# Kernel optimization log

Hardware: AMD Instinct MI355X
Metric: run time of the kernel (lower is better)

Reference implementation:

```python
import jax, jax.numpy as jnp
import numpy as np

N, C, W_DIM, H_DIM = 2, 256, 64, 64
HEADS = 4
DH = C // HEADS  # per-head dim for Q,K,V projections
EPS = 1e-5


def _layernorm(x, w, b):
    mu = jnp.mean(x, axis=-1, keepdims=True)
    var = jnp.var(x, axis=-1, keepdims=True)
    return (x - mu) * jax.lax.rsqrt(var + EPS) * w + b


def setup_inputs() -> dict:
    key = jax.random.key(0)
    ks = jax.random.split(key, 12)
    s = 1.0 / np.sqrt(C)
    return {
        "x": jax.random.normal(ks[0], (N, C, W_DIM, H_DIM), dtype=jnp.float32),
        "ln1_w": jnp.ones((C,), jnp.float32),
        "ln1_b": jnp.zeros((C,), jnp.float32),
        # per-head projection weights, laid out for x @ W: [heads, C, DH]
        "WQ": jax.random.normal(ks[1], (HEADS, C, DH), jnp.float32) * s,
        "WK": jax.random.normal(ks[2], (HEADS, C, DH), jnp.float32) * s,
        "WV": jax.random.normal(ks[3], (HEADS, C, DH), jnp.float32) * s,
        "ln2_w": jnp.ones((C,), jnp.float32),
        "ln2_b": jnp.zeros((C,), jnp.float32),
        "W1": jax.random.normal(ks[4], (C, C), jnp.float32) * s,
        "b1": jnp.zeros((C,), jnp.float32),
        "W2": jax.random.normal(ks[5], (C, C), jnp.float32) * s,
        "b2": jnp.zeros((C,), jnp.float32),
    }


def reference(x, ln1_w, ln1_b, WQ, WK, WV, ln2_w, ln2_b, W1, b1, W2, b2):
    n, c, w, h = x.shape
    s = w * h
    # 'n c w h -> n (w h) c'
    r = x.reshape(n, c, s).transpose(0, 2, 1)          # [n, s, c]
    norm = _layernorm(r, ln1_w, ln1_b)
    # all heads at once (original loops over heads)
    Q = jnp.einsum('nsc,hcd->nhsd', norm, WQ)
    K = jnp.einsum('nsc,hcd->nhsd', norm, WK)
    V = jnp.einsum('nsc,hcd->nhsd', norm, WV)
    # scale is 1/sqrt(seq_len) per original (keys.shape[1])
    y = jnp.einsum('nhqd,nhkd->nhqk', Q, K) / jnp.sqrt(jnp.float32(s))
    # QUIRK: softmax over dim=1 of [n, q, k] => the QUERY axis (axis=2 here)
    z = jax.nn.softmax(y, axis=2)
    attn = jnp.einsum('nhqk,nhkd->nhqd', z, V)         # [n, h, s, dh]
    attn_cat = attn.transpose(0, 2, 1, 3).reshape(n, s, c)
    out = attn_cat + r
    out = _layernorm(out, ln2_w, ln2_b)
    out = jax.nn.gelu(out @ W1 + b1, approximate=False) @ W2 + b2
    out = out + attn_cat
    # 'n (w h) c -> n c w h'
    return out.transpose(0, 2, 1).reshape(n, c, w, h)
```

## Files before the change

### kernel.cpp

```cpp
#include <hip/hip_runtime.h>
#include <math.h>

#define SEQ 4096
#define CH  256
#define NHT 8
#define DHD 64

#define QSCALE 0.0225421092f

using bf16x8 = __attribute__((ext_vector_type(8))) short;
using f32x4  = __attribute__((ext_vector_type(4))) float;
typedef unsigned short u16;
typedef unsigned int   u32;

__device__ __forceinline__ u16 f2bf(float f) {
    u32 u = __float_as_uint(f);
    u = (u + 0x7fffu + ((u >> 16) & 1u)) >> 16;
    return (u16)u;
}
__device__ __forceinline__ float bf2f(u16 h) {
    return __uint_as_float(((u32)h) << 16);
}
__device__ __forceinline__ float fexp2(float x) {
    return __builtin_amdgcn_exp2f(x);
}

__global__ __launch_bounds__(256) void k_prep(const float* __restrict__ x,
                                              const float* __restrict__ ln1w,
                                              const float* __restrict__ ln1b,
                                              const float* __restrict__ WQ,
                                              const float* __restrict__ WK,
                                              const float* __restrict__ WV,
                                              const float* __restrict__ W1,
                                              const float* __restrict__ W2,
                                              u16* __restrict__ norm,
                                              u16* __restrict__ BtQKV,
                                              u16* __restrict__ W1t,
                                              u16* __restrict__ W2t)
{
    __shared__ float tile[32][257];
    __shared__ float mu[32], rs[32];
    int bid = blockIdx.x;
    int t = threadIdx.x;
    if (bid < 1280) {
        int id = bid * 256 + t;
        if (id < 768 * 256) {
            int j = id >> 8, c = id & 255;
            int which = j >> 8, h = (j >> 6) & 3, d = j & 63;
            const float* W = (which == 0) ? WQ : (which == 1) ? WK : WV;
            BtQKV[id] = f2bf(W[(h * 256 + c) * 64 + d]);
        } else if (id < 768 * 256 + 65536) {
            int jj = id - 768 * 256;
            int j = jj >> 8, c = jj & 255;
            W1t[jj] = f2bf(W1[c * 256 + j]);
        } else if (id < 768 * 256 + 2 * 65536) {
            int jj = id - 768 * 256 - 65536;
            int j = jj >> 8, c = jj & 255;
            W2t[jj] = f2bf(W2[c * 256 + j]);
        }
        return;
    }
    int b2i = bid - 1280;
    int n = b2i >> 7, s0 = (b2i & 127) * 32;
    int sl = t & 31, cg = t >> 5;
    for (int cc = 0; cc < 256; cc += 8) {
        int c = cc + cg;
        tile[sl][c] = x[(n * 256 + c) * SEQ + s0 + sl];
    }
    __syncthreads();
    int wv = t >> 6, l = t & 63;
    for (int rr = 0; rr < 8; rr++) {
        int s = wv * 8 + rr;
        float a0 = tile[s][l], a1 = tile[s][l + 64], a2 = tile[s][l + 128], a3 = tile[s][l + 192];
        float sm = a0 + a1 + a2 + a3;
        float sq = a0 * a0 + a1 * a1 + a2 * a2 + a3 * a3;
        for (int off = 32; off; off >>= 1) { sm += __shfl_xor(sm, off); sq += __shfl_xor(sq, off); }
        if (l == 0) {
            float m = sm * (1.f / 256.f);
            mu[s] = m;
            rs[s] = rsqrtf(sq * (1.f / 256.f) - m * m + 1e-5f);
        }
    }
    __syncthreads();
    float ww = ln1w[t], bb = ln1b[t];
    for (int s = 0; s < 32; s++) {
        float v = (tile[s][t] - mu[s]) * rs[s] * ww + bb;
        norm[(n * SEQ + s0 + s) * 256 + t] = f2bf(v);
    }
}

__global__ __launch_bounds__(256) void k_qkv(const u16* __restrict__ norm,
                                             const u16* __restrict__ Bt,
                                             u16* __restrict__ Qo,
                                             u16* __restrict__ Ko,
                                             u16* __restrict__ Vto)
{
    int m0 = blockIdx.x * 64, j0 = blockIdx.y * 128;
    int t = threadIdx.x, w = t >> 6, lane = t & 63, quad = lane >> 4, l16 = lane & 15;
    const u16* Ap = norm + (long)(m0 + w * 16 + l16) * 256;
    const u16* Bp = Bt + (long)j0 * 256;
    f32x4 z = {0.f, 0.f, 0.f, 0.f};
    f32x4 acc[8];
    #pragma unroll
    for (int j = 0; j < 8; j++) acc[j] = z;
    #pragma unroll
    for (int kc = 0; kc < 8; kc++) {
        bf16x8 a = *(const bf16x8*)&Ap[kc * 32 + quad * 8];
        #pragma unroll
        for (int j = 0; j < 8; j++) {
            bf16x8 b = *(const bf16x8*)&Bp[(long)(j * 16 + l16) * 256 + kc * 32 + quad * 8];
            acc[j] = __builtin_amdgcn_mfma_f32_16x16x32_bf16(a, b, acc[j], 0, 0, 0);
        }
    }
    #pragma unroll
    for (int j = 0; j < 8; j++) {
        int col = j0 + j * 16 + l16;
        int which = col >> 8, h = (col >> 6) & 3, d = col & 63;
        int m = m0 + w * 16 + quad * 4;
        int n = m >> 12, s = m & 4095;
        if (which == 2) {
            u16 h0 = f2bf(acc[j][0]), h1 = f2bf(acc[j][1]);
            u16 h2_ = f2bf(acc[j][2]), h3 = f2bf(acc[j][3]);
            uint2 pk;
            pk.x = (u32)h0 | ((u32)h1 << 16);
            pk.y = (u32)h2_ | ((u32)h3 << 16);
            *(uint2*)&Vto[((long)(n * 4 + h) * 64 + d) * SEQ + s] = pk;
        } else {
            u16* dst = (which == 0) ? Qo : Ko;
            float sc = (which == 0) ? QSCALE : 1.0f;
            #pragma unroll
            for (int r = 0; r < 4; r++)
                dst[((n * 4 + h) * SEQ + s + r) * 64 + d] = f2bf(acc[j][r] * sc);
        }
    }
}

__global__ __launch_bounds__(256) void k_pass1(const u16* __restrict__ Q,
                                               const u16* __restrict__ Km,
                                               float* __restrict__ D4)
{
    __shared__ float Dred[128];
    int nh = blockIdx.y, k0 = blockIdx.x * 128, qc = blockIdx.z;
    const u16* Qh = Q + (long)nh * SEQ * 64;
    const u16* Kh = Km + (long)nh * SEQ * 64;
    int t = threadIdx.x, w = t >> 6, lane = t & 63, quad = lane >> 4, l16 = lane & 15;
    bf16x8 Kf[8][2];
    #pragma unroll
    for (int i = 0; i < 8; i++) {
        Kf[i][0] = *(const bf16x8*)&Kh[(k0 + i * 16 + l16) * 64 + quad * 8];
        Kf[i][1] = *(const bf16x8*)&Kh[(k0 + i * 16 + l16) * 64 + 32 + quad * 8];
    }
    if (t < 128) Dred[t] = 0.f;
    f32x4 z = {0.f, 0.f, 0.f, 0.f};
    float Dacc[8][4] = {};
    const int qw0 = qc * 1024 + w * 256;
    bf16x8 b0 = *(const bf16x8*)&Qh[(qw0 + l16) * 64 + quad * 8];
    bf16x8 b1 = *(const bf16x8*)&Qh[(qw0 + l16) * 64 + 32 + quad * 8];
    for (int step = 0; step < 16; step++) {
        int q = qw0 + step * 16;
        bf16x8 n0, n1;
        if (step < 15) {
            n0 = *(const bf16x8*)&Qh[(q + 16 + l16) * 64 + quad * 8];
            n1 = *(const bf16x8*)&Qh[(q + 16 + l16) * 64 + 32 + quad * 8];
        }
        #pragma unroll
        for (int i = 0; i < 8; i++) {
            f32x4 acc = z;
            acc = __builtin_amdgcn_mfma_f32_16x16x32_bf16(Kf[i][0], b0, acc, 0, 0, 0);
            acc = __builtin_amdgcn_mfma_f32_16x16x32_bf16(Kf[i][1], b1, acc, 0, 0, 0);
            #pragma unroll
            for (int r = 0; r < 4; r++) Dacc[i][r] += fexp2(acc[r]);
        }
        b0 = n0; b1 = n1;
    }
    #pragma unroll
    for (int i = 0; i < 8; i++)
        #pragma unroll
        for (int r = 0; r < 4; r++) {
            float v = Dacc[i][r];
            v += __shfl_xor(v, 1); v += __shfl_xor(v, 2);
            v += __shfl_xor(v, 4); v += __shfl_xor(v, 8);
            Dacc[i][r] = v;
        }
    __syncthreads();
    if (l16 == 0) {
        #pragma unroll
        for (int i = 0; i < 8; i++)
            #pragma unroll
            for (int r = 0; r < 4; r++)
                atomicAdd(&Dred[i * 16 + quad * 4 + r], Dacc[i][r]);
    }
    __syncthreads();
    if (t < 128) D4[((long)(qc * NHT + nh)) * SEQ + k0 + t] = Dred[t];
}

__global__ __launch_bounds__(256) void k_pass2(const u16* __restrict__ Q,
                                               const u16* __restrict__ Km,
                                               const u16* __restrict__ Vt,
                                               const float* __restrict__ D4,
                                               float* __restrict__ acat2)
{
    __shared__ __align__(16) unsigned char smem[34816];
    u16 (*lP)[64][36] = (u16(*)[64][36])smem;
    float* Lk = (float*)(smem + 18432);
    float (*SA)[68] = (float(*)[68])smem;
    float (*SB)[68] = (float(*)[68])(smem + 17408);

    int nh = blockIdx.y, q0 = blockIdx.x * 64, kcid = blockIdx.z;
    int n = nh >> 2, h = nh & 3;
    const u16* Qh = Q + (long)nh * SEQ * 64;
    const u16* Kh = Km + (long)nh * SEQ * 64;
    const u16* Vh = Vt + (long)nh * 64 * SEQ;
    int t = threadIdx.x, w = t >> 6, lane = t & 63, quad = lane >> 4, l16 = lane & 15;
    const int kw0 = kcid * 2048 + w * 512;
    const int klw = w * 512;

    {
        const float* Dp = D4 + (long)nh * SEQ + kcid * 2048;
        const long QS = (long)NHT * SEQ;
        #pragma unroll
        for (int off = 0; off < 8; off++) {
            int kl = off * 256 + t;
            float s = Dp[kl] + Dp[QS + kl] + Dp[2 * QS + kl] + Dp[3 * QS + kl];
            Lk[kl] = __log2f(s);
        }
    }
    bf16x8 Qf[4][2];
    #pragma unroll
    for (int jq = 0; jq < 4; jq++)
        #pragma unroll
        for (int ch = 0; ch < 2; ch++)
            Qf[jq][ch] = *(const bf16x8*)&Qh[(q0 + jq * 16 + l16) * 64 + ch * 32 + quad * 8];
    bf16x8 kA[2][2];
    #pragma unroll
    for (int ksub = 0; ksub < 2; ksub++) {
        kA[ksub][0] = *(const bf16x8*)&Kh[(kw0 + ksub * 16 + l16) * 64 + quad * 8];
        kA[ksub][1] = *(const bf16x8*)&Kh[(kw0 + ksub * 16 + l16) * 64 + 32 + quad * 8];
    }
    f32x4 z = {0.f, 0.f, 0.f, 0.f};
    f32x4 accO[4][4];
    #pragma unroll
    for (int jq = 0; jq < 4; jq++)
        #pragma unroll
        for (int jd = 0; jd < 4; jd++) accO[jq][jd] = z;
    __syncthreads();

    uint2 pk[2][4];
    {
        f32x4 Lv[2];
        #pragma unroll
        for (int ksub = 0; ksub < 2; ksub++)
            Lv[ksub] = *(const f32x4*)&Lk[klw + ksub * 16 + quad * 4];
        #pragma unroll
        for (int ksub = 0; ksub < 2; ksub++)
            #pragma unroll
            for (int jq = 0; jq < 4; jq++) {
                f32x4 acc = z;
                acc = __builtin_amdgcn_mfma_f32_16x16x32_bf16(kA[ksub][0], Qf[jq][0], acc, 0, 0, 0);
                acc = __builtin_amdgcn_mfma_f32_16x16x32_bf16(kA[ksub][1], Qf[jq][1], acc, 0, 0, 0);
                u32 e0 = __float_as_uint(fexp2(acc[0] - Lv[ksub][0]));
                u32 e1 = __float_as_uint(fexp2(acc[1] - Lv[ksub][1]));
                u32 e2 = __float_as_uint(fexp2(acc[2] - Lv[ksub][2]));
                u32 e3 = __float_as_uint(fexp2(acc[3] - Lv[ksub][3]));
                pk[ksub][jq].x = __builtin_amdgcn_perm(e1, e0, 0x07060302u);
                pk[ksub][jq].y = __builtin_amdgcn_perm(e3, e2, 0x07060302u);
            }
    }
    #pragma unroll
    for (int ksub = 0; ksub < 2; ksub++) {
        kA[ksub][0] = *(const bf16x8*)&Kh[(kw0 + 32 + ksub * 16 + l16) * 64 + quad * 8];
        kA[ksub][1] = *(const bf16x8*)&Kh[(kw0 + 32 + ksub * 16 + l16) * 64 + 32 + quad * 8];
    }
    bf16x8 vb[4];
    #pragma unroll
    for (int jd = 0; jd < 4; jd++)
        vb[jd] = *(const bf16x8*)&Vh[(jd * 16 + l16) * SEQ + kw0 + quad * 8];

    for (int i = 0; i < 16; i++) {
        int k0 = kw0 + i * 32;
        #pragma unroll
        for (int ksub = 0; ksub < 2; ksub++)
            #pragma unroll
            for (int jq = 0; jq < 4; jq++)
                *(uint2*)&lP[w][jq * 16 + l16][ksub * 16 + quad * 4] = pk[ksub][jq];
        if (i < 15) {
            f32x4 Lv[2];
            #pragma unroll
            for (int ksub = 0; ksub < 2; ksub++)
                Lv[ksub] = *(const f32x4*)&Lk[klw + (i + 1) * 32 + ksub * 16 + quad * 4];
            #pragma unroll
            for (int ksub = 0; ksub < 2; ksub++)
                #pragma unroll
                for (int jq = 0; jq < 4; jq++) {
                    f32x4 acc = z;
                    acc = __builtin_amdgcn_mfma_f32_16x16x32_bf16(kA[ksub][0], Qf[jq][0], acc, 0, 0, 0);
                    acc = __builtin_amdgcn_mfma_f32_16x16x32_bf16(kA[ksub][1], Qf[jq][1], acc, 0, 0, 0);
                    u32 e0 = __float_as_uint(fexp2(acc[0] - Lv[ksub][0]));
                    u32 e1 = __float_as_uint(fexp2(acc[1] - Lv[ksub][1]));
                    u32 e2 = __float_as_uint(fexp2(acc[2] - Lv[ksub][2]));
                    u32 e3 = __float_as_uint(fexp2(acc[3] - Lv[ksub][3]));
                    pk[ksub][jq].x = __builtin_amdgcn_perm(e1, e0, 0x07060302u);
                    pk[ksub][jq].y = __builtin_amdgcn_perm(e3, e2, 0x07060302u);
                }
            if (i < 14) {
                #pragma unroll
                for (int ksub = 0; ksub < 2; ksub++) {
                    kA[ksub][0] = *(const bf16x8*)&Kh[(k0 + 64 + ksub * 16 + l16) * 64 + quad * 8];
                    kA[ksub][1] = *(const bf16x8*)&Kh[(k0 + 64 + ksub * 16 + l16) * 64 + 32 + quad * 8];
                }
            }
        }
        #pragma unroll
        for (int jq = 0; jq < 4; jq++) {
            bf16x8 pa = *(const bf16x8*)&lP[w][jq * 16 + l16][quad * 8];
            #pragma unroll
            for (int jd = 0; jd < 4; jd++)
                accO[jq][jd] = __builtin_amdgcn_mfma_f32_16x16x32_bf16(pa, vb[jd], accO[jq][jd], 0, 0, 0);
        }
        if (i < 15) {
            #pragma unroll
            for (int jd = 0; jd < 4; jd++)
                vb[jd] = *(const bf16x8*)&Vh[(jd * 16 + l16) * SEQ + k0 + 32 + quad * 8];
        }
    }
    __syncthreads();
    if (w >= 2) {
        float (*S)[68] = (w == 2) ? SA : SB;
        #pragma unroll
        for (int jq = 0; jq < 4; jq++)
            #pragma unroll
            for (int jd = 0; jd < 4; jd++)
                #pragma unroll
                for (int r = 0; r < 4; r++)
                    S[jq * 16 + quad * 4 + r][jd * 16 + l16] = accO[jq][jd][r];
    }
    __syncthreads();
    if (w < 2) {
        float (*S)[68] = (w == 0) ? SA : SB;
        #pragma unroll
        for (int jq = 0; jq < 4; jq++)
            #pragma unroll
            for (int jd = 0; jd < 4; jd++)
                #pragma unroll
                for (int r = 0; r < 4; r++) {
                    float v = accO[jq][jd][r] + S[jq * 16 + quad * 4 + r][jd * 16 + l16];
                    S[jq * 16 + quad * 4 + r][jd * 16 + l16] = v;
                }
    }
    __syncthreads();
    float* dst = acat2 + (long)kcid * 8192 * 256;
    #pragma unroll
    for (int p = 0; p < 4; p++) {
        int row = p * 16 + (t >> 4);
        int ch = (t & 15) * 4;
        float4 va = *(float4*)&SA[row][ch];
        float4 vb2 = *(float4*)&SB[row][ch];
        float4 o = make_float4(va.x + vb2.x, va.y + vb2.y, va.z + vb2.z, va.w + vb2.w);
        *(float4*)&dst[((long)n * SEQ + q0 + row) * 256 + h * 64 + ch] = o;
    }
}

__global__ __launch_bounds__(256) void k_tail(const float* __restrict__ x,
                                              const float* __restrict__ acat2,
                                              const float* __restrict__ lnw,
                                              const float* __restrict__ lnb,
                                              const u16* __restrict__ W1t,
                                              const float* __restrict__ b1v,
                                              const u16* __restrict__ W2t,
                                              const float* __restrict__ b2v,
                                              float* __restrict__ out)
{
    __shared__ __align__(16) unsigned char smem[16448];
    float (*tile)[257] = (float(*)[257])smem;
    u16 (*lT)[264] = (u16(*)[264])smem;
    __shared__ float mu[16], rs[16];
    __shared__ __align__(16) u16 lH[16][264];

    const long STRIDE = (long)8192 * 256;
    int m0 = blockIdx.x * 16;
    int n = m0 >> 12, s0 = m0 & 4095;
    int t = threadIdx.x, w = t >> 6, lane = t & 63, quad = lane >> 4, l16 = lane & 15;

    {
        int sl = t & 15, cg = t >> 4;
        for (int cc = 0; cc < 256; cc += 16) {
            int c = cc + cg;
            tile[sl][c] = x[(n * 256 + c) * SEQ + s0 + sl];
        }
    }
    __syncthreads();
    for (int s = 0; s < 16; s++) {
        long idx = (long)(m0 + s) * 256 + t;
        tile[s][t] += acat2[idx] + acat2[idx + STRIDE];
    }
    __syncthreads();
    {
        int l = t & 63;
        for (int rr = 0; rr < 4; rr++) {
            int s = w * 4 + rr;
            float a0 = tile[s][l], a1 = tile[s][l + 64], a2 = tile[s][l + 128], a3 = tile[s][l + 192];
            float sm = a0 + a1 + a2 + a3;
            float sq = a0 * a0 + a1 * a1 + a2 * a2 + a3 * a3;
            for (int off = 32; off; off >>= 1) { sm += __shfl_xor(sm, off); sq += __shfl_xor(sq, off); }
            if (l == 0) {
                float m = sm * (1.f / 256.f);
                mu[s] = m;
                rs[s] = rsqrtf(sq * (1.f / 256.f) - m * m + 1e-5f);
            }
        }
    }
    __syncthreads();
    {
        float ww = lnw[t], bb = lnb[t];
        for (int s = 0; s < 16; s++)
            lH[s][t] = f2bf((tile[s][t] - mu[s]) * rs[s] * ww + bb);
    }
    __syncthreads();

    f32x4 z = {0.f, 0.f, 0.f, 0.f};
    f32x4 acc1[4];
    #pragma unroll
    for (int js = 0; js < 4; js++) acc1[js] = z;
    #pragma unroll
    for (int kc = 0; kc < 8; kc++) {
        bf16x8 b = *(const bf16x8*)&lH[l16][kc * 32 + quad * 8];
        #pragma unroll
        for (int js = 0; js < 4; js++) {
            bf16x8 a = *(const bf16x8*)&W1t[(long)(w * 64 + js * 16 + l16) * 256 + kc * 32 + quad * 8];
            acc1[js] = __builtin_amdgcn_mfma_f32_16x16x32_bf16(a, b, acc1[js], 0, 0, 0);
        }
    }
    #pragma unroll
    for (int js = 0; js < 4; js++) {
        u32 e[4];
        #pragma unroll
        for (int r = 0; r < 4; r++) {
            int j = w * 64 + js * 16 + quad * 4 + r;
            float v = acc1[js][r] + b1v[j];
            float g = 0.5f * v * (1.f + erff(v * 0.70710678118f));
            u32 u = __float_as_uint(g);
            e[r] = u + 0x7fffu + ((u >> 16) & 1u);
        }
        uint2 pk;
        pk.x = __builtin_amdgcn_perm(e[1], e[0], 0x07060302u);
        pk.y = __builtin_amdgcn_perm(e[3], e[2], 0x07060302u);
        *(uint2*)&lT[l16][w * 64 + js * 16 + quad * 4] = pk;
    }
    __syncthreads();
    f32x4 acc2[4];
    #pragma unroll
    for (int cs = 0; cs < 4; cs++) acc2[cs] = z;
    #pragma unroll
    for (int kc = 0; kc < 8; kc++) {
        bf16x8 pa = *(const bf16x8*)&lT[l16][kc * 32 + quad * 8];
        #pragma unroll
        for (int cs = 0; cs < 4; cs++) {
            bf16x8 wb = *(const bf16x8*)&W2t[(long)(w * 64 + cs * 16 + l16) * 256 + kc * 32 + quad * 8];
            acc2[cs] = __builtin_amdgcn_mfma_f32_16x16x32_bf16(pa, wb, acc2[cs], 0, 0, 0);
        }
    }
    #pragma unroll
    for (int cs = 0; cs < 4; cs++) {
        int c = w * 64 + cs * 16 + l16;
        float bj = b2v[c];
        float vv[4];
        #pragma unroll
        for (int r = 0; r < 4; r++) {
            long idx = (long)(m0 + quad * 4 + r) * 256 + c;
            vv[r] = acc2[cs][r] + bj + acat2[idx] + acat2[idx + STRIDE];
        }
        float4 o = make_float4(vv[0], vv[1], vv[2], vv[3]);
        *(float4*)&out[((long)n * 256 + c) * SEQ + s0 + quad * 4] = o;
    }
}

extern "C" void kernel_launch(void* const* d_in, const int* in_sizes, int n_in,
                              void* d_out, int out_size, void* d_ws, size_t ws_size,
                              hipStream_t stream) {
    const float* x    = (const float*)d_in[0];
    const float* ln1w = (const float*)d_in[1];
    const float* ln1b = (const float*)d_in[2];
    const float* WQ   = (const float*)d_in[3];
    const float* WK   = (const float*)d_in[4];
    const float* WV   = (const float*)d_in[5];
    const float* ln2w = (const float*)d_in[6];
    const float* ln2b = (const float*)d_in[7];
    const float* W1   = (const float*)d_in[8];
    const float* b1   = (const float*)d_in[9];
    const float* W2   = (const float*)d_in[10];
    const float* b2   = (const float*)d_in[11];
    float* out = (float*)d_out;

    char* p = (char*)d_ws;
    u16* norm   = (u16*)p;   p += (size_t)8192 * 256 * 2;
    u16* BtQKV  = (u16*)p;   p += (size_t)768 * 256 * 2;
    u16* W1t    = (u16*)p;   p += (size_t)256 * 256 * 2;
    u16* W2t    = (u16*)p;   p += (size_t)256 * 256 * 2;
    u16* Qb     = (u16*)p;   p += (size_t)NHT * SEQ * 64 * 2;
    u16* Kb     = (u16*)p;   p += (size_t)NHT * SEQ * 64 * 2;
    u16* VtT    = (u16*)p;   p += (size_t)NHT * SEQ * 64 * 2;
    float* D4   = (float*)p; p += (size_t)4 * NHT * SEQ * 4;
    float* acat2= (float*)p; p += (size_t)2 * 8192 * 256 * 4;

    k_prep<<<1536, 256, 0, stream>>>(x, ln1w, ln1b, WQ, WK, WV, W1, W2,
                                     norm, BtQKV, W1t, W2t);
    k_qkv<<<dim3(128, 6), 256, 0, stream>>>(norm, BtQKV, Qb, Kb, VtT);
    k_pass1<<<dim3(32, 8, 4), 256, 0, stream>>>(Qb, Kb, D4);
    k_pass2<<<dim3(64, 8, 2), 256, 0, stream>>>(Qb, Kb, VtT, D4, acat2);
    k_tail<<<512, 256, 0, stream>>>(x, acat2, ln2w, ln2b, W1t, b1, W2t, b2, out);
}
```

Before: 243.3 us.

## Double pass2 query tile to 128 rows and simplify software pipeline

Each k_pass2 block now processes 128 query rows instead of 64. That halves the grid and doubles reuse of every loaded K and V fragment and of the Lk values across twice as many query tiles. The software-pipelined prefetch of the next P tile is removed in favour of a straightforward compute-then-store loop. The cross-wave reduction becomes a sequential 4-step accumulation into one shared buffer. The changes raise register pressure (accO is now 8x4, Qf is 8x2) and reduce latency hiding from the dropped pipelining, and the grid shrinks to 512 blocks, with launch bounds hinting 2 blocks per CU.

```diff
diff --git a/kernel.cpp b/kernel.cpp
--- a/kernel.cpp
+++ b/kernel.cpp
@@ -194,19 +194,17 @@
     if (t < 128) D4[((long)(qc * NHT + nh)) * SEQ + k0 + t] = Dred[t];
 }
 
-__global__ __launch_bounds__(256) void k_pass2(const u16* __restrict__ Q,
-                                               const u16* __restrict__ Km,
-                                               const u16* __restrict__ Vt,
-                                               const float* __restrict__ D4,
-                                               float* __restrict__ acat2)
+__global__ __launch_bounds__(256, 2) void k_pass2(const u16* __restrict__ Q,
+                                                  const u16* __restrict__ Km,
+                                                  const u16* __restrict__ Vt,
+                                                  const float* __restrict__ D4,
+                                                  float* __restrict__ acat2)
 {
-    __shared__ __align__(16) unsigned char smem[34816];
-    u16 (*lP)[64][36] = (u16(*)[64][36])smem;
-    float* Lk = (float*)(smem + 18432);
-    float (*SA)[68] = (float(*)[68])smem;
-    float (*SB)[68] = (float(*)[68])(smem + 17408);
-
-    int nh = blockIdx.y, q0 = blockIdx.x * 64, kcid = blockIdx.z;
+    __shared__ __align__(16) u16 lP[4][128][36];
+    __shared__ float Lk[2048];
+    float (*red)[68] = (float(*)[68])lP;
+
+    int nh = blockIdx.y, q0 = blockIdx.x * 128, kcid = blockIdx.z;
     int n = nh >> 2, h = nh & 3;
     const u16* Qh = Q + (long)nh * SEQ * 64;
     const u16* Kh = Km + (long)nh * SEQ * 64;
@@ -225,9 +223,9 @@
             Lk[kl] = __log2f(s);
         }
     }
-    bf16x8 Qf[4][2];
-    #pragma unroll
-    for (int jq = 0; jq < 4; jq++)
+    bf16x8 Qf[8][2];
+    #pragma unroll
+    for (int jq = 0; jq < 8; jq++)
         #pragma unroll
         for (int ch = 0; ch < 2; ch++)
             Qf[jq][ch] = *(const bf16x8*)&Qh[(q0 + jq * 16 + l16) * 64 + ch * 32 + quad * 8];
@@ -237,81 +235,47 @@
         kA[ksub][0] = *(const bf16x8*)&Kh[(kw0 + ksub * 16 + l16) * 64 + quad * 8];
         kA[ksub][1] = *(const bf16x8*)&Kh[(kw0 + ksub * 16 + l16) * 64 + 32 + quad * 8];
     }
+    bf16x8 vb[4];
+    #pragma unroll
+    for (int jd = 0; jd < 4; jd++)
+        vb[jd] = *(const bf16x8*)&Vh[(jd * 16 + l16) * SEQ + kw0 + quad * 8];
     f32x4 z = {0.f, 0.f, 0.f, 0.f};
-    f32x4 accO[4][4];
-    #pragma unroll
-    for (int jq = 0; jq < 4; jq++)
+    f32x4 accO[8][4];
+    #pragma unroll
+    for (int jq = 0; jq < 8; jq++)
         #pragma unroll
         for (int jd = 0; jd < 4; jd++) accO[jq][jd] = z;
     __syncthreads();
 
-    uint2 pk[2][4];
-    {
-        f32x4 Lv[2];
-        #pragma unroll
-        for (int ksub = 0; ksub < 2; ksub++)
-            Lv[ksub] = *(const f32x4*)&Lk[klw + ksub * 16 + quad * 4];
-        #pragma unroll
-        for (int ksub = 0; ksub < 2; ksub++)
-            #pragma unroll
-            for (int jq = 0; jq < 4; jq++) {
+    for (int i = 0; i < 16; i++) {
+        int k0 = kw0 + i * 32;
+        #pragma unroll
+        for (int ksub = 0; ksub < 2; ksub++) {
+            f32x4 Lv = *(const f32x4*)&Lk[klw + i * 32 + ksub * 16 + quad * 4];
+            #pragma unroll
+            for (int jq = 0; jq < 8; jq++) {
                 f32x4 acc = z;
                 acc = __builtin_amdgcn_mfma_f32_16x16x32_bf16(kA[ksub][0], Qf[jq][0], acc, 0, 0, 0);
                 acc = __builtin_amdgcn_mfma_f32_16x16x32_bf16(kA[ksub][1], Qf[jq][1], acc, 0, 0, 0);
-                u32 e0 = __float_as_uint(fexp2(acc[0] - Lv[ksub][0]));
-                u32 e1 = __float_as_uint(fexp2(acc[1] - Lv[ksub][1]));
-                u32 e2 = __float_as_uint(fexp2(acc[2] - Lv[ksub][2]));
-                u32 e3 = __float_as_uint(fexp2(acc[3] - Lv[ksub][3]));
-                pk[ksub][jq].x = __builtin_amdgcn_perm(e1, e0, 0x07060302u);
-                pk[ksub][jq].y = __builtin_amdgcn_perm(e3, e2, 0x07060302u);
+                u32 e0 = __float_as_uint(fexp2(acc[0] - Lv[0]));
+                u32 e1 = __float_as_uint(fexp2(acc[1] - Lv[1]));
+                u32 e2 = __float_as_uint(fexp2(acc[2] - Lv[2]));
+                u32 e3 = __float_as_uint(fexp2(acc[3] - Lv[3]));
+                uint2 pk;
+                pk.x = __builtin_amdgcn_perm(e1, e0, 0x07060302u);
+                pk.y = __builtin_amdgcn_perm(e3, e2, 0x07060302u);
+                *(uint2*)&lP[w][jq * 16 + l16][ksub * 16 + quad * 4] = pk;
             }
-    }
-    #pragma unroll
-    for (int ksub = 0; ksub < 2; ksub++) {
-        kA[ksub][0] = *(const bf16x8*)&Kh[(kw0 + 32 + ksub * 16 + l16) * 64 + quad * 8];
-        kA[ksub][1] = *(const bf16x8*)&Kh[(kw0 + 32 + ksub * 16 + l16) * 64 + 32 + quad * 8];
-    }
-    bf16x8 vb[4];
-    #pragma unroll
-    for (int jd = 0; jd < 4; jd++)
-        vb[jd] = *(const bf16x8*)&Vh[(jd * 16 + l16) * SEQ + kw0 + quad * 8];
-
-    for (int i = 0; i < 16; i++) {
-        int k0 = kw0 + i * 32;
-        #pragma unroll
-        for (int ksub = 0; ksub < 2; ksub++)
-            #pragma unroll
-            for (int jq = 0; jq < 4; jq++)
-                *(uint2*)&lP[w][jq * 16 + l16][ksub * 16 + quad * 4] = pk[ksub][jq];
+        }
         if (i < 15) {
-            f32x4 Lv[2];
-            #pragma unroll
-            for (int ksub = 0; ksub < 2; ksub++)
-                Lv[ksub] = *(const f32x4*)&Lk[klw + (i + 1) * 32 + ksub * 16 + quad * 4];
-            #pragma unroll
-            for (int ksub = 0; ksub < 2; ksub++)
-                #pragma unroll
-                for (int jq = 0; jq < 4; jq++) {
-                    f32x4 acc = z;
-                    acc = __builtin_amdgcn_mfma_f32_16x16x32_bf16(kA[ksub][0], Qf[jq][0], acc, 0, 0, 0);
-                    acc = __builtin_amdgcn_mfma_f32_16x16x32_bf16(kA[ksub][1], Qf[jq][1], acc, 0, 0, 0);
-                    u32 e0 = __float_as_uint(fexp2(acc[0] - Lv[ksub][0]));
-                    u32 e1 = __float_as_uint(fexp2(acc[1] - Lv[ksub][1]));
-                    u32 e2 = __float_as_uint(fexp2(acc[2] - Lv[ksub][2]));
-                    u32 e3 = __float_as_uint(fexp2(acc[3] - Lv[ksub][3]));
-                    pk[ksub][jq].x = __builtin_amdgcn_perm(e1, e0, 0x07060302u);
-                    pk[ksub][jq].y = __builtin_amdgcn_perm(e3, e2, 0x07060302u);
-                }
-            if (i < 14) {
-                #pragma unroll
-                for (int ksub = 0; ksub < 2; ksub++) {
-                    kA[ksub][0] = *(const bf16x8*)&Kh[(k0 + 64 + ksub * 16 + l16) * 64 + quad * 8];
-                    kA[ksub][1] = *(const bf16x8*)&Kh[(k0 + 64 + ksub * 16 + l16) * 64 + 32 + quad * 8];
-                }
+            #pragma unroll
+            for (int ksub = 0; ksub < 2; ksub++) {
+                kA[ksub][0] = *(const bf16x8*)&Kh[(k0 + 32 + ksub * 16 + l16) * 64 + quad * 8];
+                kA[ksub][1] = *(const bf16x8*)&Kh[(k0 + 32 + ksub * 16 + l16) * 64 + 32 + quad * 8];
             }
         }
         #pragma unroll
-        for (int jq = 0; jq < 4; jq++) {
+        for (int jq = 0; jq < 8; jq++) {
             bf16x8 pa = *(const bf16x8*)&lP[w][jq * 16 + l16][quad * 8];
             #pragma unroll
             for (int jd = 0; jd < 4; jd++)
@@ -324,38 +288,27 @@
         }
     }
     __syncthreads();
-    if (w >= 2) {
-        float (*S)[68] = (w == 2) ? SA : SB;
-        #pragma unroll
-        for (int jq = 0; jq < 4; jq++)
-            #pragma unroll
-            for (int jd = 0; jd < 4; jd++)
+    for (int src = 0; src < 4; src++) {
+        if (w == src) {
+            #pragma unroll
+            for (int jq = 0; jq < 8; jq++)
                 #pragma unroll
-                for (int r = 0; r < 4; r++)
-                    S[jq * 16 + quad * 4 + r][jd * 16 + l16] = accO[jq][jd][r];
-    }
-    __syncthreads();
-    if (w < 2) {
-        float (*S)[68] = (w == 0) ? SA : SB;
-        #pragma unroll
-        for (int jq = 0; jq < 4; jq++)
-            #pragma unroll
-            for (int jd = 0; jd < 4; jd++)
-                #pragma unroll
-                for (int r = 0; r < 4; r++) {
-                    float v = accO[jq][jd][r] + S[jq * 16 + quad * 4 + r][jd * 16 + l16];
-                    S[jq * 16 + quad * 4 + r][jd * 16 + l16] = v;
-                }
-    }
-    __syncthreads();
+                for (int jd = 0; jd < 4; jd++)
+                    #pragma unroll
+                    for (int r = 0; r < 4; r++) {
+                        float* cell = &red[jq * 16 + quad * 4 + r][jd * 16 + l16];
+                        if (src == 0) *cell = accO[jq][jd][r];
+                        else          *cell += accO[jq][jd][r];
+                    }
+        }
+        __syncthreads();
+    }
     float* dst = acat2 + (long)kcid * 8192 * 256;
     #pragma unroll
-    for (int p = 0; p < 4; p++) {
+    for (int p = 0; p < 8; p++) {
         int row = p * 16 + (t >> 4);
         int ch = (t & 15) * 4;
-        float4 va = *(float4*)&SA[row][ch];
-        float4 vb2 = *(float4*)&SB[row][ch];
-        float4 o = make_float4(va.x + vb2.x, va.y + vb2.y, va.z + vb2.z, va.w + vb2.w);
+        float4 o = *(float4*)&red[row][ch];
         *(float4*)&dst[((long)n * SEQ + q0 + row) * 256 + h * 64 + ch] = o;
     }
 }
@@ -506,6 +459,6 @@
                                      norm, BtQKV, W1t, W2t);
     k_qkv<<<dim3(128, 6), 256, 0, stream>>>(norm, BtQKV, Qb, Kb, VtT);
     k_pass1<<<dim3(32, 8, 4), 256, 0, stream>>>(Qb, Kb, D4);
-    k_pass2<<<dim3(64, 8, 2), 256, 0, stream>>>(Qb, Kb, VtT, D4, acat2);
+    k_pass2<<<dim3(32, 8, 2), 256, 0, stream>>>(Qb, Kb, VtT, D4, acat2);
     k_tail<<<512, 256, 0, stream>>>(x, acat2, ln2w, ln2b, W1t, b1, W2t, b2, out);
 }
```

After: 243.7 us. No clear change (+0.2%).
